# Performance work log

Measured on AMD Instinct MI355X. Metric: run time of the kernel, lower is better.

Reference implementation:

```python
import jax, jax.numpy as jnp
import numpy as np
from jax import lax

IMG = 224
KS = 7
NS = 7
PAD = (KS // 2) * 2  # 6, max_scale=2


def _windows():
    # Replicates COGV1.__init__ geometry (torch.linspace + int truncation)
    scales = np.linspace(2.0, 1.0, NS, dtype=np.float32)
    borders = np.linspace(0, IMG // 2, NS + 1).astype(int)
    wins = []
    for s in range(NS):
        a = int(borders[s]); b = int(borders[s + 1])
        c = IMG - b; d = IMG - a
        # top, left, bottom, right windows of the hollow square
        for (t, l, bo, r) in [(a, a, b, c), (b, a, d, b), (c, b, d, d), (a, c, c, d)]:
            h = bo - t; w = r - l
            # padded window size / scale, truncated toward zero (torch .int())
            sh = int(np.float32(h + 2 * PAD) / scales[s])
            sw = int(np.float32(w + 2 * PAD) / scales[s])
            wins.append((t, l, bo, r, h, w, sh, sw))
    return wins

WINS = _windows()


def _nearest_up(f, H, W):
    # torch nearest: src_idx = floor(dst_idx * in / out); static indices
    hin, win = f.shape[-2], f.shape[-1]
    ih = (np.arange(H) * hin) // H
    iw = (np.arange(W) * win) // W
    return f[..., ih[:, None], iw[None, :]]


def _bn(x, g, b, eps=1e-5):
    # training-mode BatchNorm2d: per-batch biased stats over (N,H,W)
    m = jnp.mean(x, axis=(0, 2, 3), keepdims=True)
    v = jnp.mean((x - m) ** 2, axis=(0, 2, 3), keepdims=True)
    return (x - m) * lax.rsqrt(v + eps) * g[:, None, None] + b[:, None, None]


def _conv(x, w, padding):
    return lax.conv_general_dilated(x, w, (1, 1), padding,
                                    dimension_numbers=('NCHW', 'OIHW', 'NCHW'))


def setup_inputs() -> dict:
    key = jax.random.key(0)
    ks = jax.random.split(key, 3)
    B = 16
    return {
        'inp': jax.random.normal(ks[0], (B, 3, IMG, IMG), jnp.float32),
        'conv1_w': jax.random.normal(ks[1], (128, 3, KS, KS), jnp.float32) * 0.05,
        'gamma1': jnp.ones((128,), jnp.float32),
        'beta1': jnp.zeros((128,), jnp.float32),
        'conv2_w': jax.random.normal(ks[2], (128, 128, 3, 3), jnp.float32) * 0.05,
        'gamma2': jnp.ones((128,), jnp.float32),
        'beta2': jnp.zeros((128,), jnp.float32),
    }


def reference(inp, conv1_w, gamma1, beta1, conv2_w, gamma2, beta2):
    B = inp.shape[0]
    xp = jnp.pad(inp, ((0, 0), (0, 0), (PAD, PAD), (PAD, PAD)))  # ConstantPad2d(6)
    out = jnp.zeros((B, 128, IMG, IMG), inp.dtype)
    for (t, l, bo, r, h, w, sh, sw) in WINS:
        win = xp[:, :, t:bo + 2 * PAD, l:r + 2 * PAD]
        # antialiased bilinear downsample (== torch bilinear antialias=True)
        xd = jax.image.resize(win, (B, 3, sh, sw), method='linear', antialias=True)
        f = _conv(xd, conv1_w, 'VALID')  # 7x7 valid conv
        out = out.at[:, :, t:bo, l:r].set(_nearest_up(f, h, w))
    x = jax.nn.relu(_bn(out, gamma1, beta1))
    # MaxPool2d(kernel=3, stride=2, padding=1): 224 -> 112
    x = lax.reduce_window(x, -jnp.inf, lax.max, (1, 1, 3, 3), (1, 1, 2, 2),
                          ((0, 0), (0, 0), (1, 1), (1, 1)))
    x = _conv(x, conv2_w, ((1, 1), (1, 1)))  # 3x3 same conv
    return jax.nn.relu(_bn(x, gamma2, beta2))
```

## Files before the change

### kernel.cpp

```cpp
#include <hip/hip_runtime.h>
#include <stdint.h>

#define NW 28
#define IMG 224
#define XD_TOTAL 1822272
#define POOL_ELEMS 26615808
#define OUT_ELEMS 25690112

#define XD_OFF_B    0
#define POOL_OFF_B  3644928
#define W1P_OFF_B   56876544
#define W2T_OFF_B   56925696
#define STATS_OFF_B 57220608
#define TAB_OUT_OFF_B 93667328

typedef __attribute__((ext_vector_type(8))) short short8;
typedef __attribute__((ext_vector_type(4))) float f32x4;

#define WIN_TABLE(W) \
  W(  0,  0, 16,208, 14,110,       0,        0,    0, 7) \
  W( 16,  0,208, 16,110, 14,   73920,  1703936,  112, 7) \
  W(208, 16, 16,208, 14,110,  147840,  3407872,  224, 7) \
  W(  0,208,208, 16,110, 14,  221760,  5111808,  336, 7) \
  W( 16, 16, 16,176, 15,102,  295680,  6815744,  448, 7) \
  W( 32, 16,176, 16,102, 15,  369120,  8585216,  560, 7) \
  W(192, 32, 16,176, 15,102,  442560, 10354688,  672, 7) \
  W( 16,192,176, 16,102, 15,  516000, 12124160,  784, 7) \
  W( 32, 32, 16,144, 16, 93,  589440, 13893632,  896, 7) \
  W( 48, 32,144, 16, 93, 16,  660864, 15675392, 1008, 7) \
  W(176, 48, 16,144, 16, 93,  732288, 17457152, 1120, 7) \
  W( 32,176,144, 16, 93, 16,  803712, 19238912, 1232, 7) \
  W( 48, 48, 16,112, 18, 82,  875136, 21020672, 1344, 8) \
  W( 64, 48,112, 16, 82, 18,  945984, 22888448, 1472, 8) \
  W(160, 64, 16,112, 18, 82, 1016832, 24756224, 1600, 8) \
  W( 48,160,112, 16, 82, 18, 1087680, 26624000, 1728, 8) \
  W( 64, 64, 16, 80, 21, 69, 1158528, 28491776, 1856, 8) \
  W( 80, 64, 80, 16, 69, 21, 1228080, 30427136, 1984, 8) \
  W(144, 80, 16, 80, 21, 69, 1297632, 32362496, 2112, 8) \
  W( 64,144, 80, 16, 69, 21, 1367184, 34297856, 2240, 8) \
  W( 80, 80, 16, 48, 24, 51, 1436736, 36233216, 2368, 7) \
  W( 96, 80, 48, 16, 51, 24, 1495488, 37892096, 2480, 7) \
  W(128, 96, 16, 48, 24, 51, 1554240, 39550976, 2592, 7) \
  W( 80,128, 48, 16, 51, 24, 1612992, 41209856, 2704, 7) \
  W( 96, 96, 16, 16, 28, 28, 1671744, 42868736, 2816, 4) \
  W(112, 96, 16, 16, 28, 28, 1709376, 43859968, 2880, 4) \
  W(112,112, 16, 16, 28, 28, 1747008, 44851200, 2944, 4) \
  W( 96,112, 16, 16, 28, 28, 1784640, 45842432, 3008, 4)

#define GT(t,l,h,ww,sh,sw,xdo,fo,ts,tpb) (t),
#define GL(t,l,h,ww,sh,sw,xdo,fo,ts,tpb) (l),
#define GH(t,l,h,ww,sh,sw,xdo,fo,ts,tpb) (h),
#define GW(t,l,h,ww,sh,sw,xdo,fo,ts,tpb) (ww),
#define GSH(t,l,h,ww,sh,sw,xdo,fo,ts,tpb) (sh),
#define GSW(t,l,h,ww,sh,sw,xdo,fo,ts,tpb) (sw),
#define GXO(t,l,h,ww,sh,sw,xdo,fo,ts,tpb) (xdo),
#define GFO(t,l,h,ww,sh,sw,xdo,fo,ts,tpb) (fo),
#define GTS(t,l,h,ww,sh,sw,xdo,fo,ts,tpb) (ts),
#define GTPB(t,l,h,ww,sh,sw,xdo,fo,ts,tpb) (tpb),
#define GXE(t,l,h,ww,sh,sw,xdo,fo,ts,tpb) ((xdo) + 48*(sh)*(sw)),
#define GTE(t,l,h,ww,sh,sw,xdo,fo,ts,tpb) ((ts) + 16*(tpb)),
#define GIH(t,l,h,ww,sh,sw,xdo,fo,ts,tpb) (1.0f/(float)(h)),
#define GIW(t,l,h,ww,sh,sw,xdo,fo,ts,tpb) (1.0f/(float)(ww)),
#define GIFW(t,l,h,ww,sh,sw,xdo,fo,ts,tpb) (1.0f/(float)((sw)-6)),
#define GRSY(t,l,h,ww,sh,sw,xdo,fo,ts,tpb) ((float)((h)+12)/(float)(sh)),
#define GRSX(t,l,h,ww,sh,sw,xdo,fo,ts,tpb) ((float)((ww)+12)/(float)(sw)),
#define GI3(t,l,h,ww,sh,sw,xdo,fo,ts,tpb) (1.0f/(float)(3*(sh)*(sw))),
#define GISS(t,l,h,ww,sh,sw,xdo,fo,ts,tpb) (1.0f/(float)((sh)*(sw))),
#define GISW(t,l,h,ww,sh,sw,xdo,fo,ts,tpb) (1.0f/(float)(sw)),

__constant__ int   W_T[NW]     = { WIN_TABLE(GT) };
__constant__ int   W_L[NW]     = { WIN_TABLE(GL) };
__constant__ int   W_H[NW]     = { WIN_TABLE(GH) };
__constant__ int   W_WW[NW]    = { WIN_TABLE(GW) };
__constant__ int   W_SH[NW]    = { WIN_TABLE(GSH) };
__constant__ int   W_SW[NW]    = { WIN_TABLE(GSW) };
__constant__ int   W_XDOFF[NW] = { WIN_TABLE(GXO) };
__constant__ int   W_FOFF[NW]  = { WIN_TABLE(GFO) };
__constant__ int   W_TSTART[NW]= { WIN_TABLE(GTS) };
__constant__ int   W_TPB[NW]   = { WIN_TABLE(GTPB) };
__constant__ int   W_XDEND[NW] = { WIN_TABLE(GXE) };
__constant__ int   W_TEND[NW]  = { WIN_TABLE(GTE) };
__constant__ float W_INVH[NW]  = { WIN_TABLE(GIH) };
__constant__ float W_INVW[NW]  = { WIN_TABLE(GIW) };
__constant__ float W_INVFW[NW] = { WIN_TABLE(GIFW) };
__constant__ float W_RSY[NW]   = { WIN_TABLE(GRSY) };
__constant__ float W_RSX[NW]   = { WIN_TABLE(GRSX) };
__constant__ float W_INV3[NW]  = { WIN_TABLE(GI3) };
__constant__ float W_INVSS[NW] = { WIN_TABLE(GISS) };
__constant__ float W_INVSW[NW] = { WIN_TABLE(GISW) };

__device__ __forceinline__ float bf2f(uint16_t h) {
  union { uint32_t u; float f; } v; v.u = ((uint32_t)h) << 16; return v.f;
}
__device__ __forceinline__ uint16_t f2bf(float x) {
  union { float f; uint32_t u; } v; v.f = x;
  uint32_t r = v.u + 0x7FFFu + ((v.u >> 16) & 1u);
  return (uint16_t)(r >> 16);
}

__global__ void k_prep(const float* __restrict__ w1, const float* __restrict__ w2,
                       uint16_t* __restrict__ w1p, uint16_t* __restrict__ w2t) {
  int i = blockIdx.x * 256 + threadIdx.x;
  if (i < 128 * 192) {
    int cout = i / 192, k = i - cout * 192;
    int chunk = k >> 3, kx = k & 7;
    float v = 0.f;
    if (chunk < 21 && kx < 7) {
      int ch = chunk / 7, ky = chunk - ch * 7;
      v = w1[((cout * 3 + ch) * 7 + ky) * 7 + kx];
    }
    w1p[i] = f2bf(v);
  }
  int j = i - 128 * 192;
  if (j >= 0 && j < 128 * 1152) {
    int cout = j / 1152, k = j - cout * 1152;
    int tap = k >> 7, ci = k & 127;
    int ty = tap / 3, tx = tap - ty * 3;
    w2t[j] = f2bf(w2[((cout * 128 + ci) * 3 + ty) * 3 + tx]);
  }
}

__global__ void k_tapoff(int2* __restrict__ tab) {
  int i = blockIdx.x * 256 + threadIdx.x;
  if (i >= IMG * IMG) return;
  int y = i / IMG, x = i - y * IMG;
  int dmin = min(min(y, 223 - y), min(x, 223 - x));
  int s = dmin >> 4; if (s > 6) s = 6;
  int b2 = (s << 4) + 16, cc = 208 - (s << 4);
  int side;
  if (y < b2) side = (x < cc) ? 0 : 3;
  else if (y >= cc) side = (x >= b2) ? 2 : 1;
  else side = (x < b2) ? 1 : 3;
  int w = (s << 2) + side;
  int fh = W_SH[w] - 6, fw = W_SW[w] - 6;
  int fy = (int)(((float)((y - W_T[w]) * fh) + 0.5f) * W_INVH[w]);
  int fx = (int)(((float)((x - W_L[w]) * fw) + 0.5f) * W_INVW[w]);
  tab[i] = make_int2(W_FOFF[w] + (fy * fw + fx) * 128, fh * fw * 128);
}

__global__ void k_resize(const float* __restrict__ inp, uint16_t* __restrict__ xd) {
  int idx = blockIdx.x * 256 + threadIdx.x;
  if (idx >= XD_TOTAL) return;
  int w = 0;
  while (w < NW - 1 && idx >= W_XDEND[w]) w++;
  int rem = idx - W_XDOFF[w];
  int sh = W_SH[w], sw = W_SW[w];
  int shsw = sh * sw;
  int b  = (int)(((float)rem + 0.5f) * W_INV3[w]);
  int r2 = rem - b * 3 * shsw;
  int ch = (int)(((float)r2 + 0.5f) * W_INVSS[w]);
  int r3 = r2 - ch * shsw;
  int oy = (int)(((float)r3 + 0.5f) * W_INVSW[w]);
  int ox = r3 - oy * sw;
  int t = W_T[w], l = W_L[w], h = W_H[w], ww = W_WW[w];
  int hiny = h + 12, hinx = ww + 12;
  float rsy = W_RSY[w], rsx = W_RSX[w];
  float iky = 1.0f / rsy, ikx = 1.0f / rsx;
  float sfy = ((float)oy + 0.5f) * rsy - 0.5f;
  float sfx = ((float)ox + 0.5f) * rsx - 0.5f;
  int y0 = (int)ceilf(sfy - rsy); if (y0 < 0) y0 = 0;
  int y1 = (int)floorf(sfy + rsy); if (y1 > hiny - 1) y1 = hiny - 1;
  int x0 = (int)ceilf(sfx - rsx); if (x0 < 0) x0 = 0;
  int x1 = (int)floorf(sfx + rsx); if (x1 > hinx - 1) x1 = hinx - 1;
  float wy[4], wx[4], sy = 0.f, sx = 0.f;
  #pragma unroll
  for (int k = 0; k < 4; k++) {
    int iy = y0 + k;
    float a = (iy <= y1) ? fmaxf(0.f, 1.f - fabsf((float)iy - sfy) * iky) : 0.f;
    wy[k] = a; sy += a;
    int ix = x0 + k;
    float a2 = (ix <= x1) ? fmaxf(0.f, 1.f - fabsf((float)ix - sfx) * ikx) : 0.f;
    wx[k] = a2; sx += a2;
  }
  const float* src = inp + (b * 3 + ch) * IMG * IMG;
  float accv = 0.f;
  #pragma unroll
  for (int ky = 0; ky < 4; ky++) {
    int gy = t + y0 + ky - 6;
    if (wy[ky] > 0.f && gy >= 0 && gy < IMG) {
      float rowa = 0.f;
      #pragma unroll
      for (int kx = 0; kx < 4; kx++) {
        int gx = l + x0 + kx - 6;
        if (wx[kx] > 0.f && gx >= 0 && gx < IMG)
          rowa += wx[kx] * src[gy * IMG + gx];
      }
      accv += wy[ky] * rowa;
    }
  }
  xd[idx] = f2bf(accv / (sy * sx));
}

__global__ void k_conv1(const uint16_t* __restrict__ xd,
                        const uint16_t* __restrict__ w1p,
                        uint16_t* __restrict__ f) {
  __shared__ short8 As[512];
  __shared__ short8 Bs[512];
  int bid = blockIdx.x;
  int w = 0;
  while (w < NW - 1 && bid >= W_TEND[w]) w++;
  int rel = bid - W_TSTART[w];
  int tpb = W_TPB[w];
  int b  = rel / tpb;
  int mt = rel - b * tpb;
  int m0 = mt << 7;
  int sh = W_SH[w], sw = W_SW[w];
  int fh = sh - 6, fw = sw - 6;
  int fhfw = fh * fw;
  float invfw = W_INVFW[w];
  int xdo = W_XDOFF[w];
  int fo  = W_FOFF[w];
  int tid = threadIdx.x;
  int lane = tid & 63, wv = tid >> 6;
  int mn = tid & 127, q0 = tid >> 7;

  int pm0 = m0 + mn; if (pm0 > fhfw - 1) pm0 = fhfw - 1;
  int fy0 = (int)(((float)pm0 + 0.5f) * invfw);
  int fx0 = pm0 - fy0 * fw;
  const uint16_t* arow = xd + xdo + (b * 3) * sh * sw;
  const uint16_t* brow = w1p + mn * 192;

  f32x4 acc[4][4];
  #pragma unroll
  for (int i = 0; i < 4; i++)
    #pragma unroll
    for (int j = 0; j < 4; j++)
      acc[i][j] = (f32x4){0.f, 0.f, 0.f, 0.f};

  for (int kk = 0; kk < 6; kk++) {
    short8 av[2], bv[2];
    #pragma unroll
    for (int j = 0; j < 2; j++) {
      int q = (j << 1) | q0;
      int gc = (kk << 2) + q;
      const uint16_t* src;
      if (gc < 21) {
        int ch = gc / 7, ky = gc - ch * 7;
        src = arow + (ch * sh + fy0 + ky) * sw + fx0;
      } else {
        src = xd;
      }
      short8 pk;
      pk[0]=(short)src[0]; pk[1]=(short)src[1]; pk[2]=(short)src[2]; pk[3]=(short)src[3];
      pk[4]=(short)src[4]; pk[5]=(short)src[5]; pk[6]=(short)src[6]; pk[7]=(short)src[7];
      av[j] = pk;
      bv[j] = *(const short8*)(brow + (kk << 5) + (q << 3));
    }
    __syncthreads();
    #pragma unroll
    for (int j = 0; j < 2; j++) {
      int ck = (j << 8) + tid;
      As[ck] = av[j];
      Bs[ck] = bv[j];
    }
    __syncthreads();
    int q = lane >> 4, ln = lane & 15;
    int wmB = (wv >> 1) << 6, wnB = (wv & 1) << 6;
    short8 af[4], bfr[4];
    #pragma unroll
    for (int i = 0; i < 4; i++) af[i]  = As[(q << 7) + wmB + (i << 4) + ln];
    #pragma unroll
    for (int j = 0; j < 4; j++) bfr[j] = Bs[(q << 7) + wnB + (j << 4) + ln];
    #pragma unroll
    for (int i = 0; i < 4; i++)
      #pragma unroll
      for (int j = 0; j < 4; j++)
        acc[i][j] = __builtin_amdgcn_mfma_f32_16x16x32_bf16(af[i], bfr[j], acc[i][j], 0, 0, 0);
  }

  int q = lane >> 4, ln = lane & 15;
  int wmB = (wv >> 1) << 6, wnB = (wv & 1) << 6;
  int base = fo + b * fhfw * 128;
  #pragma unroll
  for (int i = 0; i < 4; i++) {
    #pragma unroll
    for (int j = 0; j < 4; j++) {
      int n = wnB + (j << 4) + ln;
      int mrow = m0 + wmB + (i << 4) + (q << 2);
      #pragma unroll
      for (int r = 0; r < 4; r++) {
        int pm = mrow + r;
        if (pm < fhfw) f[base + pm * 128 + n] = f2bf(acc[i][j][r]);
      }
    }
  }
}

__global__ void k_stats1(const uint16_t* __restrict__ f, float* __restrict__ sums) {
  __shared__ float cwt[960];
  __shared__ float sS[128], sQ[128];
  int w = blockIdx.x;
  int b = blockIdx.y;
  int sh = W_SH[w], sw = W_SW[w];
  int fh = sh - 6, fw = sw - 6, fhfw = fh * fw;
  int h = W_H[w], ww = W_WW[w];
  int tid = threadIdx.x;
  if (tid < 128) { sS[tid] = 0.f; sQ[tid] = 0.f; }
  for (int e = tid; e < fhfw; e += 1024) {
    int fy = e / fw, fx = e - fy * fw;
    int cy = ((fy + 1) * h + fh - 1) / fh - (fy * h + fh - 1) / fh;
    int cx = ((fx + 1) * ww + fw - 1) / fw - (fx * ww + fw - 1) / fw;
    cwt[e] = (float)(cy * cx);
  }
  __syncthreads();
  int c = tid & 127, eh = tid >> 7;
  int base = W_FOFF[w] + b * fhfw * 128;
  float s = 0.f, q2 = 0.f;
  for (int e = eh; e < fhfw; e += 8) {
    float v = bf2f(f[base + e * 128 + c]);
    float cw = cwt[e];
    s += v * cw; q2 += v * v * cw;
  }
  atomicAdd(&sS[c], s);
  atomicAdd(&sQ[c], q2);
  __syncthreads();
  if (tid < 128) {
    atomicAdd(&sums[tid], sS[tid]);
    atomicAdd(&sums[128 + tid], sQ[tid]);
  }
}

__global__ void k_bnparam(const float* __restrict__ sums,
                          const float* __restrict__ gamma, const float* __restrict__ beta,
                          float n, float* __restrict__ scale, float* __restrict__ bias) {
  int c = threadIdx.x;
  float mean = sums[c] / n;
  float var = sums[128 + c] / n - mean * mean;
  var = fmaxf(var, 0.f);
  float sc = gamma[c] / sqrtf(var + 1e-5f);
  scale[c] = sc;
  bias[c] = beta[c] - mean * sc;
}

__global__ void k_maxpool(const uint16_t* __restrict__ f,
                          const float* __restrict__ scale, const float* __restrict__ bias,
                          const int2* __restrict__ tab,
                          uint16_t* __restrict__ pooled) {
  int tid = threadIdx.x;
  int g = blockIdx.x * 16 + (tid >> 4);
  int c0 = (tid & 15) << 3;
  int xx = g % 114;
  int r  = g / 114;
  int yy = r % 114;
  int bb = r / 114;
  short8 outv = (short8){0,0,0,0,0,0,0,0};
  if (yy >= 1 && yy <= 112 && xx >= 1 && xx <= 112) {
    float m[8];
    #pragma unroll
    for (int k = 0; k < 8; k++) m[k] = -1e30f;
    int py = yy - 1, px = xx - 1;
    #pragma unroll
    for (int dy = 0; dy < 3; dy++) {
      int y = 2 * py - 1 + dy;
      if (y < 0) continue;
      #pragma unroll
      for (int dx = 0; dx < 3; dx++) {
        int x = 2 * px - 1 + dx;
        if (x < 0) continue;
        int2 t = tab[y * IMG + x];
        short8 v = *(const short8*)(f + t.x + bb * t.y + c0);
        #pragma unroll
        for (int k = 0; k < 8; k++) m[k] = fmaxf(m[k], bf2f((uint16_t)v[k]));
      }
    }
    f32x4 s0 = *(const f32x4*)(scale + c0);
    f32x4 s1 = *(const f32x4*)(scale + c0 + 4);
    f32x4 b0 = *(const f32x4*)(bias + c0);
    f32x4 b1 = *(const f32x4*)(bias + c0 + 4);
    #pragma unroll
    for (int k = 0; k < 4; k++) {
      outv[k]     = (short)f2bf(fmaxf(m[k]     * s0[k] + b0[k], 0.f));
      outv[k + 4] = (short)f2bf(fmaxf(m[k + 4] * s1[k] + b1[k], 0.f));
    }
  }
  *(short8*)(pooled + (size_t)g * 128 + c0) = outv;
}

__global__ void k_conv2(const uint16_t* __restrict__ pooled,
                        const uint16_t* __restrict__ w2t,
                        float* __restrict__ out, float* __restrict__ sums) {
  __shared__ short8 As[1024];
  __shared__ short8 Bs[1024];
  __shared__ float sS[128], sQ[128];
  int bid = blockIdx.x;
  int b = bid / 98;
  int m0 = bid << 7;
  int local0 = m0 - b * 12544;
  int tid = threadIdx.x;
  int lane = tid & 63, wv = tid >> 6;
  int mn = tid & 127, q0 = tid >> 7;
  int loc = local0 + mn;
  int yp = loc / 112;
  int xp = loc - yp * 112;
  const uint16_t* ap = pooled + (size_t)b * 114 * 114 * 128;
  const uint16_t* brow = w2t + mn * 1152;
  if (tid < 128) { sS[tid] = 0.f; sQ[tid] = 0.f; }

  f32x4 acc[4][4];
  #pragma unroll
  for (int i = 0; i < 4; i++)
    #pragma unroll
    for (int j = 0; j < 4; j++)
      acc[i][j] = (f32x4){0.f, 0.f, 0.f, 0.f};

  for (int s = 0; s < 18; s++) {
    short8 av[2][2], bv[2][2];
    #pragma unroll
    for (int u = 0; u < 2; u++) {
      int kk = (s << 1) + u;
      int tap = kk >> 2;
      int c0 = (kk & 3) << 5;
      int ty = tap / 3, tx = tap - ty * 3;
      #pragma unroll
      for (int j = 0; j < 2; j++) {
        int q = (j << 1) | q0;
        av[u][j] = *(const short8*)(ap + (((yp + ty) * 114) + xp + tx) * 128 + c0 + (q << 3));
        bv[u][j] = *(const short8*)(brow + (kk << 5) + (q << 3));
      }
    }
    __syncthreads();
    #pragma unroll
    for (int u = 0; u < 2; u++)
      #pragma unroll
      for (int j = 0; j < 2; j++) {
        int ck = (u << 9) + (j << 8) + tid;
        As[ck] = av[u][j];
        Bs[ck] = bv[u][j];
      }
    __syncthreads();
    int q = lane >> 4, ln = lane & 15;
    int wmB = (wv >> 1) << 6, wnB = (wv & 1) << 6;
    #pragma unroll
    for (int u = 0; u < 2; u++) {
      short8 af[4], bfr[4];
      #pragma unroll
      for (int i = 0; i < 4; i++) af[i]  = As[(u << 9) + (q << 7) + wmB + (i << 4) + ln];
      #pragma unroll
      for (int j = 0; j < 4; j++) bfr[j] = Bs[(u << 9) + (q << 7) + wnB + (j << 4) + ln];
      #pragma unroll
      for (int i = 0; i < 4; i++)
        #pragma unroll
        for (int j = 0; j < 4; j++)
          acc[i][j] = __builtin_amdgcn_mfma_f32_16x16x32_bf16(af[i], bfr[j], acc[i][j], 0, 0, 0);
    }
  }

  int q = lane >> 4, ln = lane & 15;
  int wmB = (wv >> 1) << 6, wnB = (wv & 1) << 6;
  #pragma unroll
  for (int i = 0; i < 4; i++) {
    #pragma unroll
    for (int j = 0; j < 4; j++) {
      int n = wnB + (j << 4) + ln;
      int prow = local0 + wmB + (i << 4) + (q << 2);
      float* dst = out + (size_t)(b * 128 + n) * 12544 + prow;
      *(f32x4*)dst = acc[i][j];
    }
  }
  #pragma unroll
  for (int j = 0; j < 4; j++) {
    int n = wnB + (j << 4) + ln;
    float s = 0.f, q2 = 0.f;
    #pragma unroll
    for (int i = 0; i < 4; i++)
      #pragma unroll
      for (int r = 0; r < 4; r++) {
        float v = acc[i][j][r];
        s += v; q2 += v * v;
      }
    atomicAdd(&sS[n], s);
    atomicAdd(&sQ[n], q2);
  }
  __syncthreads();
  if (tid < 128) {
    atomicAdd(&sums[tid], sS[tid]);
    atomicAdd(&sums[128 + tid], sQ[tid]);
  }
}

__global__ void k_final(f32x4* __restrict__ out,
                        const float* __restrict__ scale, const float* __restrict__ bias) {
  int i = blockIdx.x * 256 + threadIdx.x;
  int c = (i / 3136) & 127;
  f32x4 v = out[i];
  float sc = scale[c], bi = bias[c];
  #pragma unroll
  for (int k = 0; k < 4; k++) v[k] = fmaxf(v[k] * sc + bi, 0.f);
  out[i] = v;
}

extern "C" void kernel_launch(void* const* d_in, const int* in_sizes, int n_in,
                              void* d_out, int out_size, void* d_ws, size_t ws_size,
                              hipStream_t stream) {
  (void)in_sizes; (void)n_in; (void)out_size; (void)ws_size;
  const float* inp = (const float*)d_in[0];
  const float* w1  = (const float*)d_in[1];
  const float* g1  = (const float*)d_in[2];
  const float* b1  = (const float*)d_in[3];
  const float* w2  = (const float*)d_in[4];
  const float* g2  = (const float*)d_in[5];
  const float* b2  = (const float*)d_in[6];
  float* out = (float*)d_out;
  char* ws = (char*)d_ws;
  uint16_t* xd     = (uint16_t*)(ws + XD_OFF_B);
  uint16_t* pooled = (uint16_t*)(ws + POOL_OFF_B);
  uint16_t* w1p    = (uint16_t*)(ws + W1P_OFF_B);
  uint16_t* w2t    = (uint16_t*)(ws + W2T_OFF_B);
  float* stats  = (float*)(ws + STATS_OFF_B);
  int2*  tab    = (int2*)((char*)d_out + TAB_OUT_OFF_B);
  float* sums1  = stats;
  float* sums2  = stats + 256;
  float* scale1 = stats + 512;
  float* bias1  = stats + 640;
  float* scale2 = stats + 768;
  float* bias2  = stats + 896;
  uint16_t* f = (uint16_t*)d_out;

  hipMemsetAsync(stats, 0, 2048, stream);
  k_prep   <<<dim3(672),        dim3(256),  0, stream>>>(w1, w2, w1p, w2t);
  k_tapoff <<<dim3(196),        dim3(256),  0, stream>>>(tab);
  k_resize <<<dim3(7119),       dim3(256),  0, stream>>>(inp, xd);
  k_conv1  <<<dim3(3072),       dim3(256),  0, stream>>>(xd, w1p, f);
  k_stats1 <<<dim3(28, 16),     dim3(1024), 0, stream>>>(f, sums1);
  k_bnparam<<<dim3(1),          dim3(128),  0, stream>>>(sums1, g1, b1, 802816.0f, scale1, bias1);
  k_maxpool<<<dim3(12996),      dim3(256),  0, stream>>>(f, scale1, bias1, tab, pooled);
  k_conv2  <<<dim3(1568),       dim3(256),  0, stream>>>(pooled, w2t, out, sums2);
  k_bnparam<<<dim3(1),          dim3(128),  0, stream>>>(sums2, g2, b2, 200704.0f, scale2, bias2);
  k_final  <<<dim3(25088),      dim3(256),  0, stream>>>((f32x4*)out, scale2, bias2);
}
```

Baseline: 461.1 us.

## Load conv2 MFMA fragments directly from global, pre-swizzle weights, drop LDS staging

New measurement: 494.9 us. 1.07x slower.

```diff
diff --git a/kernel.cpp b/kernel.cpp
--- a/kernel.cpp
+++ b/kernel.cpp
@@ -99,7 +99,7 @@
 }
 
 __global__ void k_prep(const float* __restrict__ w1, const float* __restrict__ w2,
-                       uint16_t* __restrict__ w1p, uint16_t* __restrict__ w2t) {
+                       uint16_t* __restrict__ w1p, uint16_t* __restrict__ w2f) {
   int i = blockIdx.x * 256 + threadIdx.x;
   if (i < 128 * 192) {
     int cout = i / 192, k = i - cout * 192;
@@ -111,12 +111,18 @@
     }
     w1p[i] = f2bf(v);
   }
-  int j = i - 128 * 192;
-  if (j >= 0 && j < 128 * 1152) {
-    int cout = j / 1152, k = j - cout * 1152;
+  int j2 = i - 128 * 192;
+  if (j2 >= 0 && j2 < 128 * 1152) {
+    int e    = j2 & 7;
+    int lane = (j2 >> 3) & 63;
+    int jj   = (j2 >> 9) & 3;
+    int half = (j2 >> 11) & 1;
+    int kk   = j2 >> 12;
+    int cout = half * 64 + jj * 16 + (lane & 15);
+    int k    = kk * 32 + ((lane >> 4) << 3) + e;
     int tap = k >> 7, ci = k & 127;
     int ty = tap / 3, tx = tap - ty * 3;
-    w2t[j] = f2bf(w2[((cout * 128 + ci) * 3 + ty) * 3 + tx]);
+    w2f[j2] = f2bf(w2[((cout * 128 + ci) * 3 + ty) * 3 + tx]);
   }
 }
 
@@ -377,10 +383,8 @@
 }
 
 __global__ void k_conv2(const uint16_t* __restrict__ pooled,
-                        const uint16_t* __restrict__ w2t,
+                        const uint16_t* __restrict__ w2f,
                         float* __restrict__ out, float* __restrict__ sums) {
-  __shared__ short8 As[1024];
-  __shared__ short8 Bs[1024];
   __shared__ float sS[128], sQ[128];
   int bid = blockIdx.x;
   int b = bid / 98;
@@ -388,13 +392,20 @@
   int local0 = m0 - b * 12544;
   int tid = threadIdx.x;
   int lane = tid & 63, wv = tid >> 6;
-  int mn = tid & 127, q0 = tid >> 7;
-  int loc = local0 + mn;
-  int yp = loc / 112;
-  int xp = loc - yp * 112;
+  int q = lane >> 4, ln = lane & 15;
+  int wmB = (wv >> 1) << 6;
+  int half = wv & 1;
+  int wnB = half << 6;
+  if (tid < 128) { sS[tid] = 0.f; sQ[tid] = 0.f; }
+
   const uint16_t* ap = pooled + (size_t)b * 114 * 114 * 128;
-  const uint16_t* brow = w2t + mn * 1152;
-  if (tid < 128) { sS[tid] = 0.f; sQ[tid] = 0.f; }
+  int rowoff[4];
+  #pragma unroll
+  for (int i = 0; i < 4; i++) {
+    int pm = local0 + wmB + (i << 4) + ln;
+    int yp = pm / 112, xp = pm - yp * 112;
+    rowoff[i] = (yp * 114 + xp) * 128;
+  }
 
   f32x4 acc[4][4];
   #pragma unroll
@@ -403,40 +414,23 @@
     for (int j = 0; j < 4; j++)
       acc[i][j] = (f32x4){0.f, 0.f, 0.f, 0.f};
 
-  for (int s = 0; s < 18; s++) {
-    short8 av[2][2], bv[2][2];
-    #pragma unroll
-    for (int u = 0; u < 2; u++) {
-      int kk = (s << 1) + u;
-      int tap = kk >> 2;
-      int c0 = (kk & 3) << 5;
-      int ty = tap / 3, tx = tap - ty * 3;
-      #pragma unroll
-      for (int j = 0; j < 2; j++) {
-        int q = (j << 1) | q0;
-        av[u][j] = *(const short8*)(ap + (((yp + ty) * 114) + xp + tx) * 128 + c0 + (q << 3));
-        bv[u][j] = *(const short8*)(brow + (kk << 5) + (q << 3));
-      }
-    }
-    __syncthreads();
-    #pragma unroll
-    for (int u = 0; u < 2; u++)
-      #pragma unroll
-      for (int j = 0; j < 2; j++) {
-        int ck = (u << 9) + (j << 8) + tid;
-        As[ck] = av[u][j];
-        Bs[ck] = bv[u][j];
-      }
-    __syncthreads();
-    int q = lane >> 4, ln = lane & 15;
-    int wmB = (wv >> 1) << 6, wnB = (wv & 1) << 6;
-    #pragma unroll
-    for (int u = 0; u < 2; u++) {
+  const uint16_t* bbase = w2f + (half << 11) + (lane << 3);
+
+  #pragma unroll
+  for (int tap = 0; tap < 9; tap++) {
+    const int ty = tap / 3, tx = tap - ty * 3;
+    int tbase = (ty * 114 + tx) * 128 + (q << 3);
+    #pragma unroll
+    for (int cc = 0; cc < 4; cc++) {
+      int kk = (tap << 2) + cc;
+      int c0 = cc << 5;
       short8 af[4], bfr[4];
       #pragma unroll
-      for (int i = 0; i < 4; i++) af[i]  = As[(u << 9) + (q << 7) + wmB + (i << 4) + ln];
-      #pragma unroll
-      for (int j = 0; j < 4; j++) bfr[j] = Bs[(u << 9) + (q << 7) + wnB + (j << 4) + ln];
+      for (int i = 0; i < 4; i++)
+        af[i] = *(const short8*)(ap + rowoff[i] + tbase + c0);
+      #pragma unroll
+      for (int j = 0; j < 4; j++)
+        bfr[j] = *(const short8*)(bbase + (kk << 12) + (j << 9));
       #pragma unroll
       for (int i = 0; i < 4; i++)
         #pragma unroll
@@ -445,8 +439,6 @@
     }
   }
 
-  int q = lane >> 4, ln = lane & 15;
-  int wmB = (wv >> 1) << 6, wnB = (wv & 1) << 6;
   #pragma unroll
   for (int i = 0; i < 4; i++) {
     #pragma unroll
@@ -457,6 +449,7 @@
       *(f32x4*)dst = acc[i][j];
     }
   }
+  __syncthreads();
   #pragma unroll
   for (int j = 0; j < 4; j++) {
     int n = wnB + (j << 4) + ln;
@@ -505,7 +498,7 @@
   uint16_t* xd     = (uint16_t*)(ws + XD_OFF_B);
   uint16_t* pooled = (uint16_t*)(ws + POOL_OFF_B);
   uint16_t* w1p    = (uint16_t*)(ws + W1P_OFF_B);
-  uint16_t* w2t    = (uint16_t*)(ws + W2T_OFF_B);
+  uint16_t* w2f    = (uint16_t*)(ws + W2T_OFF_B);
   float* stats  = (float*)(ws + STATS_OFF_B);
   int2*  tab    = (int2*)((char*)d_out + TAB_OUT_OFF_B);
   float* sums1  = stats;
@@ -517,14 +510,14 @@
   uint16_t* f = (uint16_t*)d_out;
 
   hipMemsetAsync(stats, 0, 2048, stream);
-  k_prep   <<<dim3(672),        dim3(256),  0, stream>>>(w1, w2, w1p, w2t);
+  k_prep   <<<dim3(672),        dim3(256),  0, stream>>>(w1, w2, w1p, w2f);
   k_tapoff <<<dim3(196),        dim3(256),  0, stream>>>(tab);
   k_resize <<<dim3(7119),       dim3(256),  0, stream>>>(inp, xd);
   k_conv1  <<<dim3(3072),       dim3(256),  0, stream>>>(xd, w1p, f);
   k_stats1 <<<dim3(28, 16),     dim3(1024), 0, stream>>>(f, sums1);
   k_bnparam<<<dim3(1),          dim3(128),  0, stream>>>(sums1, g1, b1, 802816.0f, scale1, bias1);
   k_maxpool<<<dim3(12996),      dim3(256),  0, stream>>>(f, scale1, bias1, tab, pooled);
-  k_conv2  <<<dim3(1568),       dim3(256),  0, stream>>>(pooled, w2t, out, sums2);
+  k_conv2  <<<dim3(1568),       dim3(256),  0, stream>>>(pooled, w2f, out, sums2);
   k_bnparam<<<dim3(1),          dim3(128),  0, stream>>>(sums2, g2, b2, 200704.0f, scale2, bias2);
   k_final  <<<dim3(25088),      dim3(256),  0, stream>>>((f32x4*)out, scale2, bias2);
 }
```
